# Optimization experiments

Hardware: AMD Instinct MI355X
Metric: run time of the kernel (lower is better)

The kernel has to match this reference:

```python
import jax, jax.numpy as jnp
import numpy as np

D_MODEL = 1024
N_HEADS = 16
SEQ = 2048
BATCH = 2


def setup_inputs() -> dict:
    key = jax.random.key(0)
    ks = jax.random.split(key, 12)
    s = 1.0 / np.sqrt(D_MODEL)
    return {
        "q_input": jax.random.normal(ks[0], (BATCH, SEQ, D_MODEL), jnp.float32),
        "k_input": jax.random.normal(ks[1], (BATCH, SEQ, D_MODEL), jnp.float32),
        "v_input": jax.random.normal(ks[2], (BATCH, SEQ, D_MODEL), jnp.float32),
        "key_padding_mask": jnp.zeros((BATCH, SEQ), dtype=bool),
        "wq": jax.random.normal(ks[3], (D_MODEL, D_MODEL), jnp.float32) * s,
        "bq": jnp.zeros((D_MODEL,), jnp.float32),
        "wk": jax.random.normal(ks[4], (D_MODEL, D_MODEL), jnp.float32) * s,
        "bk": jnp.zeros((D_MODEL,), jnp.float32),
        "wv": jax.random.normal(ks[5], (D_MODEL, D_MODEL), jnp.float32) * s,
        "bv": jnp.zeros((D_MODEL,), jnp.float32),
        "wo": jax.random.normal(ks[6], (D_MODEL, D_MODEL), jnp.float32) * s,
        "bo": jnp.zeros((D_MODEL,), jnp.float32),
    }


def reference(q_input, k_input, v_input, key_padding_mask, wq, bq, wk, bk, wv, bv, wo, bo):
    B, Lq, _ = q_input.shape
    Lk = k_input.shape[1]
    d_head = D_MODEL // N_HEADS
    # torch Linear: x @ W.T + b
    Q = q_input @ wq.T + bq
    K = k_input @ wk.T + bk
    V = v_input @ wv.T + bv
    # [B, H, L, d_head]
    Qh = Q.reshape(B, Lq, N_HEADS, d_head).transpose(0, 2, 1, 3)
    Kh = K.reshape(B, Lk, N_HEADS, d_head).transpose(0, 2, 1, 3)
    Vh = V.reshape(B, Lk, N_HEADS, d_head).transpose(0, 2, 1, 3)
    scores = jnp.einsum("bhqd,bhkd->bhqk", Qh, Kh) / jnp.sqrt(jnp.float32(d_head))
    # causal mask (use_mask=True)
    causal = jnp.arange(Lk)[None, :] > jnp.arange(Lq)[:, None]  # [Lq, Lk]
    scores = jnp.where(causal[None, None], -jnp.inf, scores)
    # key padding mask [B,1,1,Lk]
    scores = jnp.where(key_padding_mask[:, None, None, :], -jnp.inf, scores)
    # module's global all-inf fallback (scalar condition)
    probs = jnp.where(
        jnp.all(jnp.isinf(scores)),
        jnp.full_like(scores, 1.0 / Lk),
        jax.nn.softmax(scores, axis=-1),
    )
    # dropout is identity in eval mode
    out = jnp.einsum("bhqk,bhkd->bhqd", probs, Vh)
    out = out.transpose(0, 2, 1, 3).reshape(B, Lq, D_MODEL)
    return out @ wo.T + bo
```

## Files before the change

### kernel.cpp

```cpp
#include <hip/hip_runtime.h>
#include <cstdint>
#include <cstddef>

#define DM   1024
#define HEADS 16
#define DH    64
#define SEQL  2048
#define BATCH 2
#define MTOT  (BATCH*SEQL)

typedef __attribute__((ext_vector_type(8))) short short8;
typedef __attribute__((ext_vector_type(4))) float floatx4;

__device__ __forceinline__ unsigned short f2bf(float f) {
  unsigned int u = __float_as_uint(f);
  u = (u + 0x7FFFu + ((u >> 16) & 1u)) >> 16;
  return (unsigned short)u;
}

__device__ __forceinline__ void async_ld16(const void* g, void* l) {
  __builtin_amdgcn_global_load_lds(
      (const __attribute__((address_space(1))) unsigned int*)g,
      (__attribute__((address_space(3))) unsigned int*)l, 16, 0, 0);
}

__global__ void cvt_bf16(const float* __restrict__ s, unsigned short* __restrict__ d, int n) {
  int i = (blockIdx.x * blockDim.x + threadIdx.x) * 4;
  if (i < n) {
    float4 v = *(const float4*)(s + i);
    ushort4 o;
    o.x = f2bf(v.x); o.y = f2bf(v.y); o.z = f2bf(v.z); o.w = f2bf(v.w);
    *(ushort4*)(d + i) = o;
  }
}

template<bool OUT_BF16>
__device__ __forceinline__ void gemm128(const unsigned short* __restrict__ A,
                                        const unsigned short* __restrict__ Bw,
                                        const float* __restrict__ bias,
                                        void* __restrict__ Cout,
                                        unsigned short* As, unsigned short* Bs) {
  const int K = DM, N = DM;
  const int m0 = blockIdx.y * 128, n0 = blockIdx.x * 128;
  const int tid  = threadIdx.x;
  const int lane = tid & 63, wvi = tid >> 6;
  const int lq = lane & 15, quad = lane >> 4;
  const int wrow = wvi >> 1, wcol = wvi & 1;

  floatx4 acc[4][4];
  #pragma unroll
  for (int i = 0; i < 4; i++)
    #pragma unroll
    for (int j = 0; j < 4; j++)
      #pragma unroll
      for (int e = 0; e < 4; e++) acc[i][j][e] = 0.0f;

  for (int kt = 0; kt < K; kt += 64) {
    #pragma unroll
    for (int cc = 0; cc < 4; cc++) {
      int c = wvi + cc * 4;
      int e = c * 512 + lane * 8;
      int r = e >> 6, col = e & 63;
      async_ld16(A  + (size_t)(m0 + r) * K + kt + col, As + c * 512);
      async_ld16(Bw + (size_t)(n0 + r) * K + kt + col, Bs + c * 512);
    }
    __syncthreads();
    #pragma unroll
    for (int ks = 0; ks < 64; ks += 32) {
      short8 af[4], bf[4];
      #pragma unroll
      for (int i = 0; i < 4; i++)
        af[i] = *(const short8*)&As[(wrow * 64 + i * 16 + lq) * 64 + ks + quad * 8];
      #pragma unroll
      for (int j = 0; j < 4; j++)
        bf[j] = *(const short8*)&Bs[(wcol * 64 + j * 16 + lq) * 64 + ks + quad * 8];
      #pragma unroll
      for (int i = 0; i < 4; i++)
        #pragma unroll
        for (int j = 0; j < 4; j++)
          acc[i][j] = __builtin_amdgcn_mfma_f32_16x16x32_bf16(af[i], bf[j], acc[i][j], 0, 0, 0);
    }
    __syncthreads();
  }

  #pragma unroll
  for (int i = 0; i < 4; i++) {
    #pragma unroll
    for (int j = 0; j < 4; j++) {
      int colg = n0 + wcol * 64 + j * 16 + lq;
      float bb = bias[colg];
      #pragma unroll
      for (int r = 0; r < 4; r++) {
        int rowg = m0 + wrow * 64 + i * 16 + quad * 4 + r;
        float v = acc[i][j][r] + bb;
        if (OUT_BF16) ((unsigned short*)Cout)[(size_t)rowg * N + colg] = f2bf(v);
        else          ((float*)Cout)[(size_t)rowg * N + colg] = v;
      }
    }
  }
}

__global__ __launch_bounds__(256, 2) void qkv_gemm(
    const unsigned short* Xq, const unsigned short* Xk, const unsigned short* Xv,
    const unsigned short* Wq, const unsigned short* Wk, const unsigned short* Wv,
    const float* bq, const float* bk, const float* bv,
    unsigned short* Qo, unsigned short* Ko, unsigned short* Vo) {
  __shared__ unsigned short As[128 * 64], Bs[128 * 64];
  const unsigned short *X, *W; const float* b; unsigned short* O;
  if (blockIdx.z == 0)      { X = Xq; W = Wq; b = bq; O = Qo; }
  else if (blockIdx.z == 1) { X = Xk; W = Wk; b = bk; O = Ko; }
  else                      { X = Xv; W = Wv; b = bv; O = Vo; }
  gemm128<true>(X, W, b, O, As, Bs);
}

__global__ __launch_bounds__(256, 2) void out_gemm(
    const unsigned short* A, const unsigned short* W, const float* b, float* C) {
  __shared__ unsigned short As[128 * 64], Bs[128 * 64];
  gemm128<false>(A, W, b, C, As, Bs);
}

__global__ void v_transpose(const unsigned short* __restrict__ Vb,
                            unsigned short* __restrict__ VT) {
  __shared__ unsigned short Ts[64 * 72];
  const int kt = blockIdx.x, h = blockIdx.y, b = blockIdx.z;
  const int tid = threadIdx.x;
  const int krow = tid >> 4, dcol = (tid & 15) * 4;
  const unsigned short* src = Vb + (size_t)(b * SEQL + kt * 64) * DM + h * DH;
  #pragma unroll
  for (int j = 0; j < 4; j++) {
    ushort4 v = *(const ushort4*)(src + (size_t)(j * 16 + krow) * DM + dcol);
    Ts[(dcol + 0) * 72 + j * 16 + krow] = v.x;
    Ts[(dcol + 1) * 72 + j * 16 + krow] = v.y;
    Ts[(dcol + 2) * 72 + j * 16 + krow] = v.z;
    Ts[(dcol + 3) * 72 + j * 16 + krow] = v.w;
  }
  __syncthreads();
  unsigned short* dst = VT + (size_t)((b * HEADS + h) * 32 + kt) * 4096;
  #pragma unroll
  for (int jj = 0; jj < 2; jj++) {
    int e = jj * 256 + tid;
    int drow = e >> 3, koff = (e & 7) * 8;
    *(short8*)(dst + drow * 64 + koff) = *(const short8*)&Ts[drow * 72 + koff];
  }
}

__global__ __launch_bounds__(256, 4) void attn_kernel(
    const unsigned short* __restrict__ Q, const unsigned short* __restrict__ K,
    const unsigned short* __restrict__ VT, const unsigned char* __restrict__ kpm,
    unsigned short* __restrict__ O) {
  __shared__ unsigned short Ks[64 * 72];
  __shared__ unsigned short VTs[64 * 72];
  __shared__ unsigned short Ps[4][16 * 72];

  const int bid = blockIdx.x;
  const int qt = 31 - (bid >> 5);
  const int bh = bid & 31;
  const int h = bh & 15, b = bh >> 4;
  const int tid = threadIdx.x, lane = tid & 63, wvi = tid >> 6;
  const int lq = lane & 15, quad = lane >> 4;
  const size_t bbase = (size_t)b * SEQL * DM;

  const int srow = tid >> 4;
  const int scol = (tid & 15) * 4;

  const unsigned short* Kg  = K + bbase + (size_t)h * DH;
  const unsigned short* VTg = VT + (size_t)(b * HEADS + h) * 32 * 4096;
  const unsigned char*  mp  = kpm + (size_t)b * SEQL;

  const unsigned short* Qrow = Q + bbase + (size_t)(qt * 64 + wvi * 16 + lq) * DM + h * DH;
  const short8 qf0 = *(const short8*)(Qrow + quad * 8);
  const short8 qf1 = *(const short8*)(Qrow + 32 + quad * 8);

  ushort4 kr[4], vr[4];
  unsigned int mr[4];
  #pragma unroll
  for (int j = 0; j < 4; j++) {
    kr[j] = *(const ushort4*)(Kg + (size_t)(j * 16 + srow) * DM + scol);
    vr[j] = *(const ushort4*)(VTg + (j * 16 + srow) * 64 + scol);
  }
  #pragma unroll
  for (int t = 0; t < 4; t++) mr[t] = *(const unsigned int*)(mp + t * 16 + quad * 4);

  float m_run = -1e30f, l_run = 0.f;
  floatx4 o[4];
  #pragma unroll
  for (int t = 0; t < 4; t++)
    #pragma unroll
    for (int e = 0; e < 4; e++) o[t][e] = 0.f;

  const float SC = 0.125f * 1.44269504088896f;

  for (int kt = 0; kt <= qt; kt++) {
    __syncthreads();
    #pragma unroll
    for (int j = 0; j < 4; j++) {
      *(ushort4*)&Ks [(j * 16 + srow) * 72 + scol] = kr[j];
      *(ushort4*)&VTs[(j * 16 + srow) * 72 + scol] = vr[j];
    }
    __syncthreads();

    unsigned int mcur[4];
    #pragma unroll
    for (int t = 0; t < 4; t++) mcur[t] = mr[t];

    if (kt < qt) {
      const int kn = kt + 1;
      #pragma unroll
      for (int j = 0; j < 4; j++) {
        kr[j] = *(const ushort4*)(Kg + (size_t)(kn * 64 + j * 16 + srow) * DM + scol);
        vr[j] = *(const ushort4*)(VTg + (size_t)kn * 4096 + (j * 16 + srow) * 64 + scol);
      }
      #pragma unroll
      for (int t = 0; t < 4; t++)
        mr[t] = *(const unsigned int*)(mp + kn * 64 + t * 16 + quad * 4);
    }

    floatx4 st[4];
    #pragma unroll
    for (int t = 0; t < 4; t++) {
      #pragma unroll
      for (int e = 0; e < 4; e++) st[t][e] = 0.f;
      const short8 a0 = *(const short8*)&Ks[(t * 16 + lq) * 72 + quad * 8];
      const short8 a1 = *(const short8*)&Ks[(t * 16 + lq) * 72 + 32 + quad * 8];
      st[t] = __builtin_amdgcn_mfma_f32_16x16x32_bf16(a0, qf0, st[t], 0, 0, 0);
      st[t] = __builtin_amdgcn_mfma_f32_16x16x32_bf16(a1, qf1, st[t], 0, 0, 0);
    }

    const bool diag = (kt == qt);
    const int qg_off = wvi * 16 + lq;
    float x[4][4];
    #pragma unroll
    for (int t = 0; t < 4; t++) {
      #pragma unroll
      for (int r = 0; r < 4; r++) {
        const int keyl = t * 16 + quad * 4 + r;
        float v = st[t][r] * SC;
        const bool msk = ((mcur[t] >> (8 * r)) & 0xffu) != 0u;
        if ((diag && keyl > qg_off) || msk) v = -1e30f;
        x[t][r] = v;
      }
    }

    float pmax = -1e30f;
    #pragma unroll
    for (int t = 0; t < 4; t++)
      #pragma unroll
      for (int r = 0; r < 4; r++) pmax = fmaxf(pmax, x[t][r]);
    pmax = fmaxf(pmax, __shfl_xor(pmax, 16));
    pmax = fmaxf(pmax, __shfl_xor(pmax, 32));
    const float mnew = fmaxf(m_run, pmax);
    const float alpha = exp2f(m_run - mnew);
    m_run = mnew;
    float psum = 0.f;
    #pragma unroll
    for (int t = 0; t < 4; t++)
      #pragma unroll
      for (int r = 0; r < 4; r++) {
        const float p = exp2f(x[t][r] - mnew);
        x[t][r] = p;
        psum += p;
      }
    psum += __shfl_xor(psum, 16);
    psum += __shfl_xor(psum, 32);
    l_run = l_run * alpha + psum;

    #pragma unroll
    for (int t = 0; t < 4; t++) {
      ushort4 w;
      w.x = f2bf(x[t][0]); w.y = f2bf(x[t][1]); w.z = f2bf(x[t][2]); w.w = f2bf(x[t][3]);
      *(ushort4*)&Ps[wvi][lq * 72 + t * 16 + quad * 4] = w;
    }

    float am[4];
    #pragma unroll
    for (int r = 0; r < 4; r++) am[r] = __shfl(alpha, quad * 20 + r);
    #pragma unroll
    for (int t = 0; t < 4; t++)
      #pragma unroll
      for (int r = 0; r < 4; r++) o[t][r] *= am[r];

    const short8 pa0 = *(const short8*)&Ps[wvi][lq * 72 + quad * 8];
    const short8 pa1 = *(const short8*)&Ps[wvi][lq * 72 + 32 + quad * 8];
    #pragma unroll
    for (int t = 0; t < 4; t++) {
      const short8 b0 = *(const short8*)&VTs[(t * 16 + lq) * 72 + quad * 8];
      const short8 b1 = *(const short8*)&VTs[(t * 16 + lq) * 72 + 32 + quad * 8];
      o[t] = __builtin_amdgcn_mfma_f32_16x16x32_bf16(pa0, b0, o[t], 0, 0, 0);
      o[t] = __builtin_amdgcn_mfma_f32_16x16x32_bf16(pa1, b1, o[t], 0, 0, 0);
    }
  }

  float linv[4];
  #pragma unroll
  for (int r = 0; r < 4; r++) linv[r] = 1.0f / __shfl(l_run, quad * 20 + r);
  #pragma unroll
  for (int t = 0; t < 4; t++)
    #pragma unroll
    for (int r = 0; r < 4; r++) {
      const int rowg = qt * 64 + wvi * 16 + quad * 4 + r;
      const int colg = h * 64 + t * 16 + lq;
      O[bbase + (size_t)rowg * DM + colg] = f2bf(o[t][r] * linv[r]);
    }
}

extern "C" void kernel_launch(void* const* d_in, const int* in_sizes, int n_in,
                              void* d_out, int out_size, void* d_ws, size_t ws_size,
                              hipStream_t stream) {
  const float* qin = (const float*)d_in[0];
  const float* kin = (const float*)d_in[1];
  const float* vin = (const float*)d_in[2];
  const unsigned char* kpm = (const unsigned char*)d_in[3];
  const float* wq = (const float*)d_in[4];
  const float* bq = (const float*)d_in[5];
  const float* wk = (const float*)d_in[6];
  const float* bk = (const float*)d_in[7];
  const float* wv = (const float*)d_in[8];
  const float* bv = (const float*)d_in[9];
  const float* wo = (const float*)d_in[10];
  const float* bo = (const float*)d_in[11];

  const size_t XN = (size_t)MTOT * DM;
  const size_t WN = (size_t)DM * DM;
  unsigned short* Xq  = (unsigned short*)d_ws;
  unsigned short* Xk  = Xq  + XN;
  unsigned short* Xv  = Xk  + XN;
  unsigned short* Wqb = Xv  + XN;
  unsigned short* Wkb = Wqb + WN;
  unsigned short* Wvb = Wkb + WN;
  unsigned short* Wob = Wvb + WN;
  unsigned short* Qb  = Wob + WN;
  unsigned short* Kb  = Qb  + XN;
  unsigned short* Vb  = Kb  + XN;
  unsigned short* Ob  = Vb  + XN;
  unsigned short* VTg = Xq;

  cvt_bf16<<<dim3((unsigned)(XN / 4 / 256)), 256, 0, stream>>>(qin, Xq, (int)XN);
  cvt_bf16<<<dim3((unsigned)(XN / 4 / 256)), 256, 0, stream>>>(kin, Xk, (int)XN);
  cvt_bf16<<<dim3((unsigned)(XN / 4 / 256)), 256, 0, stream>>>(vin, Xv, (int)XN);
  cvt_bf16<<<dim3((unsigned)(WN / 4 / 256)), 256, 0, stream>>>(wq, Wqb, (int)WN);
  cvt_bf16<<<dim3((unsigned)(WN / 4 / 256)), 256, 0, stream>>>(wk, Wkb, (int)WN);
  cvt_bf16<<<dim3((unsigned)(WN / 4 / 256)), 256, 0, stream>>>(wv, Wvb, (int)WN);
  cvt_bf16<<<dim3((unsigned)(WN / 4 / 256)), 256, 0, stream>>>(wo, Wob, (int)WN);

  dim3 g1(DM / 128, MTOT / 128, 3);
  qkv_gemm<<<g1, 256, 0, stream>>>(Xq, Xk, Xv, Wqb, Wkb, Wvb, bq, bk, bv, Qb, Kb, Vb);

  v_transpose<<<dim3(SEQL / 64, HEADS, BATCH), 256, 0, stream>>>(Vb, VTg);

  attn_kernel<<<dim3(BATCH * HEADS * (SEQL / 64)), 256, 0, stream>>>(Qb, Kb, VTg, kpm, Ob);

  dim3 g2(DM / 128, MTOT / 128, 1);
  out_gemm<<<g2, 256, 0, stream>>>(Ob, Wob, bo, (float*)d_out);
}
```

Before: 252.4 us.

## Fuse conversions, split-K output GEMM, peel causal diagonal tile in attention

```diff
diff --git a/kernel.cpp b/kernel.cpp
--- a/kernel.cpp
+++ b/kernel.cpp
@@ -24,22 +24,46 @@
       (__attribute__((address_space(3))) unsigned int*)l, 16, 0, 0);
 }
 
-__global__ void cvt_bf16(const float* __restrict__ s, unsigned short* __restrict__ d, int n) {
-  int i = (blockIdx.x * blockDim.x + threadIdx.x) * 4;
-  if (i < n) {
-    float4 v = *(const float4*)(s + i);
-    ushort4 o;
-    o.x = f2bf(v.x); o.y = f2bf(v.y); o.z = f2bf(v.z); o.w = f2bf(v.w);
-    *(ushort4*)(d + i) = o;
-  }
-}
-
-template<bool OUT_BF16>
+__global__ void cvt_all(const float* __restrict__ q, const float* __restrict__ k,
+                        const float* __restrict__ v, const float* __restrict__ w0,
+                        const float* __restrict__ w1, const float* __restrict__ w2,
+                        const float* __restrict__ w3,
+                        unsigned short* __restrict__ Xq, unsigned short* __restrict__ Xk,
+                        unsigned short* __restrict__ Xv, unsigned short* __restrict__ W0,
+                        unsigned short* __restrict__ W1, unsigned short* __restrict__ W2,
+                        unsigned short* __restrict__ W3, float* __restrict__ zout) {
+  const int bid = blockIdx.x;
+  const float* src; unsigned short* dst; int base;
+  if (bid < 12288) {
+    int seg = bid >> 12;
+    base = (bid & 4095) * 1024;
+    src = seg == 0 ? q : seg == 1 ? k : v;
+    dst = seg == 0 ? Xq : seg == 1 ? Xk : Xv;
+  } else if (bid < 16384) {
+    int b2 = bid - 12288;
+    int seg = b2 >> 10;
+    base = (b2 & 1023) * 1024;
+    src = seg == 0 ? w0 : seg == 1 ? w1 : seg == 2 ? w2 : w3;
+    dst = seg == 0 ? W0 : seg == 1 ? W1 : seg == 2 ? W2 : W3;
+  } else {
+    int i = (bid - 16384) * 1024 + threadIdx.x * 4;
+    *(float4*)(zout + i) = make_float4(0.f, 0.f, 0.f, 0.f);
+    return;
+  }
+  int i = base + threadIdx.x * 4;
+  float4 vv = *(const float4*)(src + i);
+  ushort4 o;
+  o.x = f2bf(vv.x); o.y = f2bf(vv.y); o.z = f2bf(vv.z); o.w = f2bf(vv.w);
+  *(ushort4*)(dst + i) = o;
+}
+
+template<bool OUT_BF16, bool ATOMIC>
 __device__ __forceinline__ void gemm128(const unsigned short* __restrict__ A,
                                         const unsigned short* __restrict__ Bw,
                                         const float* __restrict__ bias,
                                         void* __restrict__ Cout,
-                                        unsigned short* As, unsigned short* Bs) {
+                                        unsigned short* As, unsigned short* Bs,
+                                        int k_lo, int k_hi) {
   const int K = DM, N = DM;
   const int m0 = blockIdx.y * 128, n0 = blockIdx.x * 128;
   const int tid  = threadIdx.x;
@@ -55,7 +79,7 @@
       #pragma unroll
       for (int e = 0; e < 4; e++) acc[i][j][e] = 0.0f;
 
-  for (int kt = 0; kt < K; kt += 64) {
+  for (int kt = k_lo; kt < k_hi; kt += 64) {
     #pragma unroll
     for (int cc = 0; cc < 4; cc++) {
       int c = wvi + cc * 4;
@@ -88,19 +112,20 @@
     #pragma unroll
     for (int j = 0; j < 4; j++) {
       int colg = n0 + wcol * 64 + j * 16 + lq;
-      float bb = bias[colg];
+      float bb = bias ? bias[colg] : 0.0f;
       #pragma unroll
       for (int r = 0; r < 4; r++) {
         int rowg = m0 + wrow * 64 + i * 16 + quad * 4 + r;
         float v = acc[i][j][r] + bb;
-        if (OUT_BF16) ((unsigned short*)Cout)[(size_t)rowg * N + colg] = f2bf(v);
-        else          ((float*)Cout)[(size_t)rowg * N + colg] = v;
+        if (OUT_BF16)      ((unsigned short*)Cout)[(size_t)rowg * N + colg] = f2bf(v);
+        else if (ATOMIC)   atomicAdd(&((float*)Cout)[(size_t)rowg * N + colg], v);
+        else               ((float*)Cout)[(size_t)rowg * N + colg] = v;
       }
     }
   }
 }
 
-__global__ __launch_bounds__(256, 2) void qkv_gemm(
+__global__ __launch_bounds__(256, 3) void qkv_gemm(
     const unsigned short* Xq, const unsigned short* Xk, const unsigned short* Xv,
     const unsigned short* Wq, const unsigned short* Wk, const unsigned short* Wv,
     const float* bq, const float* bk, const float* bv,
@@ -110,13 +135,14 @@
   if (blockIdx.z == 0)      { X = Xq; W = Wq; b = bq; O = Qo; }
   else if (blockIdx.z == 1) { X = Xk; W = Wk; b = bk; O = Ko; }
   else                      { X = Xv; W = Wv; b = bv; O = Vo; }
-  gemm128<true>(X, W, b, O, As, Bs);
-}
-
-__global__ __launch_bounds__(256, 2) void out_gemm(
+  gemm128<true, false>(X, W, b, O, As, Bs, 0, DM);
+}
+
+__global__ __launch_bounds__(256, 2) void out_gemm_sk(
     const unsigned short* A, const unsigned short* W, const float* b, float* C) {
   __shared__ unsigned short As[128 * 64], Bs[128 * 64];
-  gemm128<false>(A, W, b, C, As, Bs);
+  const int klo = blockIdx.z * 512;
+  gemm128<false, true>(A, W, blockIdx.z == 0 ? b : nullptr, C, As, Bs, klo, klo + 512);
 }
 
 __global__ void v_transpose(const unsigned short* __restrict__ Vb,
@@ -163,9 +189,9 @@
   const int srow = tid >> 4;
   const int scol = (tid & 15) * 4;
 
-  const unsigned short* Kg  = K + bbase + (size_t)h * DH;
-  const unsigned short* VTg = VT + (size_t)(b * HEADS + h) * 32 * 4096;
-  const unsigned char*  mp  = kpm + (size_t)b * SEQL;
+  const unsigned short* kptr = K + bbase + (size_t)h * DH + (size_t)srow * DM + scol;
+  const unsigned short* vptr = VT + (size_t)(b * HEADS + h) * 32 * 4096 + srow * 64 + scol;
+  const unsigned char*  mptr = kpm + (size_t)b * SEQL + quad * 4;
 
   const unsigned short* Qrow = Q + bbase + (size_t)(qt * 64 + wvi * 16 + lq) * DM + h * DH;
   const short8 qf0 = *(const short8*)(Qrow + quad * 8);
@@ -175,11 +201,12 @@
   unsigned int mr[4];
   #pragma unroll
   for (int j = 0; j < 4; j++) {
-    kr[j] = *(const ushort4*)(Kg + (size_t)(j * 16 + srow) * DM + scol);
-    vr[j] = *(const ushort4*)(VTg + (j * 16 + srow) * 64 + scol);
-  }
-  #pragma unroll
-  for (int t = 0; t < 4; t++) mr[t] = *(const unsigned int*)(mp + t * 16 + quad * 4);
+    kr[j] = *(const ushort4*)(kptr + (size_t)j * 16 * DM);
+    vr[j] = *(const ushort4*)(vptr + j * 1024);
+  }
+  #pragma unroll
+  for (int t = 0; t < 4; t++) mr[t] = *(const unsigned int*)(mptr + t * 16);
+  kptr += (size_t)64 * DM; vptr += 4096; mptr += 64;
 
   float m_run = -1e30f, l_run = 0.f;
   floatx4 o[4];
@@ -189,32 +216,9 @@
     for (int e = 0; e < 4; e++) o[t][e] = 0.f;
 
   const float SC = 0.125f * 1.44269504088896f;
-
-  for (int kt = 0; kt <= qt; kt++) {
-    __syncthreads();
-    #pragma unroll
-    for (int j = 0; j < 4; j++) {
-      *(ushort4*)&Ks [(j * 16 + srow) * 72 + scol] = kr[j];
-      *(ushort4*)&VTs[(j * 16 + srow) * 72 + scol] = vr[j];
-    }
-    __syncthreads();
-
-    unsigned int mcur[4];
-    #pragma unroll
-    for (int t = 0; t < 4; t++) mcur[t] = mr[t];
-
-    if (kt < qt) {
-      const int kn = kt + 1;
-      #pragma unroll
-      for (int j = 0; j < 4; j++) {
-        kr[j] = *(const ushort4*)(Kg + (size_t)(kn * 64 + j * 16 + srow) * DM + scol);
-        vr[j] = *(const ushort4*)(VTg + (size_t)kn * 4096 + (j * 16 + srow) * 64 + scol);
-      }
-      #pragma unroll
-      for (int t = 0; t < 4; t++)
-        mr[t] = *(const unsigned int*)(mp + kn * 64 + t * 16 + quad * 4);
-    }
-
+  const int qg = wvi * 16 + lq;
+
+  auto tile_body = [&](bool diag, const unsigned int* mcur) {
     floatx4 st[4];
     #pragma unroll
     for (int t = 0; t < 4; t++) {
@@ -226,22 +230,28 @@
       st[t] = __builtin_amdgcn_mfma_f32_16x16x32_bf16(a1, qf1, st[t], 0, 0, 0);
     }
 
-    const bool diag = (kt == qt);
-    const int qg_off = wvi * 16 + lq;
     float x[4][4];
     #pragma unroll
-    for (int t = 0; t < 4; t++) {
-      #pragma unroll
-      for (int r = 0; r < 4; r++) {
-        const int keyl = t * 16 + quad * 4 + r;
-        float v = st[t][r] * SC;
-        const bool msk = ((mcur[t] >> (8 * r)) & 0xffu) != 0u;
-        if ((diag && keyl > qg_off) || msk) v = -1e30f;
-        x[t][r] = v;
-      }
-    }
-
-    float pmax = -1e30f;
+    for (int t = 0; t < 4; t++)
+      #pragma unroll
+      for (int r = 0; r < 4; r++) x[t][r] = st[t][r];
+
+    if (__any((int)((mcur[0] | mcur[1] | mcur[2] | mcur[3]) != 0u))) {
+      #pragma unroll
+      for (int t = 0; t < 4; t++)
+        #pragma unroll
+        for (int r = 0; r < 4; r++)
+          if ((mcur[t] >> (8 * r)) & 0xffu) x[t][r] = -1e33f;
+    }
+    if (diag) {
+      #pragma unroll
+      for (int t = 0; t < 4; t++)
+        #pragma unroll
+        for (int r = 0; r < 4; r++)
+          if (t * 16 + quad * 4 + r > qg) x[t][r] = -1e33f;
+    }
+
+    float pmax = -1e33f;
     #pragma unroll
     for (int t = 0; t < 4; t++)
       #pragma unroll
@@ -249,14 +259,15 @@
     pmax = fmaxf(pmax, __shfl_xor(pmax, 16));
     pmax = fmaxf(pmax, __shfl_xor(pmax, 32));
     const float mnew = fmaxf(m_run, pmax);
-    const float alpha = exp2f(m_run - mnew);
+    const float alpha = exp2f((m_run - mnew) * SC);
+    const float c = -mnew * SC;
     m_run = mnew;
     float psum = 0.f;
     #pragma unroll
     for (int t = 0; t < 4; t++)
       #pragma unroll
       for (int r = 0; r < 4; r++) {
-        const float p = exp2f(x[t][r] - mnew);
+        const float p = exp2f(fmaf(x[t][r], SC, c));
         x[t][r] = p;
         psum += p;
       }
@@ -266,9 +277,9 @@
 
     #pragma unroll
     for (int t = 0; t < 4; t++) {
-      ushort4 w;
-      w.x = f2bf(x[t][0]); w.y = f2bf(x[t][1]); w.z = f2bf(x[t][2]); w.w = f2bf(x[t][3]);
-      *(ushort4*)&Ps[wvi][lq * 72 + t * 16 + quad * 4] = w;
+      unsigned int p01 = (__float_as_uint(x[t][1]) & 0xffff0000u) | (__float_as_uint(x[t][0]) >> 16);
+      unsigned int p23 = (__float_as_uint(x[t][3]) & 0xffff0000u) | (__float_as_uint(x[t][2]) >> 16);
+      *(uint2*)&Ps[wvi][lq * 72 + t * 16 + quad * 4] = make_uint2(p01, p23);
     }
 
     float am[4];
@@ -288,7 +299,40 @@
       o[t] = __builtin_amdgcn_mfma_f32_16x16x32_bf16(pa0, b0, o[t], 0, 0, 0);
       o[t] = __builtin_amdgcn_mfma_f32_16x16x32_bf16(pa1, b1, o[t], 0, 0, 0);
     }
-  }
+  };
+
+  for (int kt = 0; kt < qt; kt++) {
+    __syncthreads();
+    #pragma unroll
+    for (int j = 0; j < 4; j++) {
+      *(ushort4*)&Ks [(j * 16 + srow) * 72 + scol] = kr[j];
+      *(ushort4*)&VTs[(j * 16 + srow) * 72 + scol] = vr[j];
+    }
+    unsigned int mcur[4];
+    #pragma unroll
+    for (int t = 0; t < 4; t++) mcur[t] = mr[t];
+    __syncthreads();
+
+    #pragma unroll
+    for (int j = 0; j < 4; j++) {
+      kr[j] = *(const ushort4*)(kptr + (size_t)j * 16 * DM);
+      vr[j] = *(const ushort4*)(vptr + j * 1024);
+    }
+    #pragma unroll
+    for (int t = 0; t < 4; t++) mr[t] = *(const unsigned int*)(mptr + t * 16);
+    kptr += (size_t)64 * DM; vptr += 4096; mptr += 64;
+
+    tile_body(false, mcur);
+  }
+
+  __syncthreads();
+  #pragma unroll
+  for (int j = 0; j < 4; j++) {
+    *(ushort4*)&Ks [(j * 16 + srow) * 72 + scol] = kr[j];
+    *(ushort4*)&VTs[(j * 16 + srow) * 72 + scol] = vr[j];
+  }
+  __syncthreads();
+  tile_body(true, mr);
 
   float linv[4];
   #pragma unroll
@@ -334,13 +378,9 @@
   unsigned short* Ob  = Vb  + XN;
   unsigned short* VTg = Xq;
 
-  cvt_bf16<<<dim3((unsigned)(XN / 4 / 256)), 256, 0, stream>>>(qin, Xq, (int)XN);
-  cvt_bf16<<<dim3((unsigned)(XN / 4 / 256)), 256, 0, stream>>>(kin, Xk, (int)XN);
-  cvt_bf16<<<dim3((unsigned)(XN / 4 / 256)), 256, 0, stream>>>(vin, Xv, (int)XN);
-  cvt_bf16<<<dim3((unsigned)(WN / 4 / 256)), 256, 0, stream>>>(wq, Wqb, (int)WN);
-  cvt_bf16<<<dim3((unsigned)(WN / 4 / 256)), 256, 0, stream>>>(wk, Wkb, (int)WN);
-  cvt_bf16<<<dim3((unsigned)(WN / 4 / 256)), 256, 0, stream>>>(wv, Wvb, (int)WN);
-  cvt_bf16<<<dim3((unsigned)(WN / 4 / 256)), 256, 0, stream>>>(wo, Wob, (int)WN);
+  cvt_all<<<dim3(20480), 256, 0, stream>>>(qin, kin, vin, wq, wk, wv, wo,
+                                           Xq, Xk, Xv, Wqb, Wkb, Wvb, Wob,
+                                           (float*)d_out);
 
   dim3 g1(DM / 128, MTOT / 128, 3);
   qkv_gemm<<<g1, 256, 0, stream>>>(Xq, Xk, Xv, Wqb, Wkb, Wvb, bq, bk, bv, Qb, Kb, Vb);
@@ -349,6 +389,6 @@
 
   attn_kernel<<<dim3(BATCH * HEADS * (SEQL / 64)), 256, 0, stream>>>(Qb, Kb, VTg, kpm, Ob);
 
-  dim3 g2(DM / 128, MTOT / 128, 1);
-  out_gemm<<<g2, 256, 0, stream>>>(Ob, Wob, bo, (float*)d_out);
-}
+  dim3 g2(DM / 128, MTOT / 128, 2);
+  out_gemm_sk<<<g2, 256, 0, stream>>>(Ob, Wob, bo, (float*)d_out);
+}
```

Result: no change. 250.5 us (-0.8%).
